# Kernel optimization log

Measured on AMD Instinct MI355X. Metric: run time of the kernel, lower is better.

Reference implementation:

```python
import jax, jax.numpy as jnp
import numpy as np

N, E, B = 50000, 200000, 64
IN_NODE, IN_EDGE = 64, 16
D_NODE, D_EDGE, HID, L = 128, 64, 64, 6


def _w(k, shape):
    # fan-in scaled init (like torch Linear default scale)
    return jax.random.normal(k, shape, jnp.float32) / np.sqrt(shape[-2]).astype(np.float32)


def setup_inputs() -> dict:
    key = jax.random.key(0)
    ks = jax.random.split(key, 16)
    return {
        "x": jax.random.normal(ks[0], (N, IN_NODE), jnp.float32),
        "edge_attr": jax.random.normal(ks[1], (E, IN_EDGE), jnp.float32),
        "edge_index": jax.random.randint(ks[2], (2, E), 0, N),
        "batch": jnp.sort(jax.random.randint(ks[3], (N,), 0, B)),
        "lin_x_w": _w(ks[4], (IN_NODE, D_NODE)), "lin_x_b": jnp.zeros((D_NODE,), jnp.float32),
        "lin_e_w": _w(ks[5], (IN_EDGE, D_EDGE)), "lin_e_b": jnp.zeros((D_EDGE,), jnp.float32),
        "msg_w": _w(ks[6], (L, D_NODE, D_EDGE)),
        "phie_w1": _w(ks[7], (L, D_EDGE + 2 * D_NODE, HID)), "phie_b1": jnp.zeros((L, HID), jnp.float32),
        "phie_w2": _w(ks[8], (L, HID, D_EDGE)), "phie_b2": jnp.zeros((L, D_EDGE), jnp.float32),
        "phiv_w1": _w(ks[9], (L, D_NODE + D_EDGE, HID)), "phiv_b1": jnp.zeros((L, HID), jnp.float32),
        "phiv_w2": _w(ks[10], (L, HID, D_NODE)), "phiv_b2": jnp.zeros((L, D_NODE), jnp.float32),
        "ro_w1": _w(ks[11], (D_NODE, D_NODE)), "ro_b1": jnp.zeros((D_NODE,), jnp.float32),
        "ro_w2": _w(ks[12], (D_NODE, D_NODE)), "ro_b2": jnp.zeros((D_NODE,), jnp.float32),
    }


def reference(x, edge_attr, edge_index, batch,
              lin_x_w, lin_x_b, lin_e_w, lin_e_b, msg_w,
              phie_w1, phie_b1, phie_w2, phie_b2,
              phiv_w1, phiv_b1, phiv_w2, phiv_b2,
              ro_w1, ro_b1, ro_w2, ro_b2):
    src, dst = edge_index[0], edge_index[1]
    n = x.shape[0]
    h = x @ lin_x_w + lin_x_b          # [N, d_node]
    e = edge_attr @ lin_e_w + lin_e_b  # [E, d_edge]
    # per-node in-degree for scatter_mean (clamped to 1, as in torch_scatter)
    deg = jnp.maximum(jax.ops.segment_sum(jnp.ones((dst.shape[0],), h.dtype), dst, num_segments=n), 1.0)[:, None]

    def step(carry, p):
        h, e = carry
        mw, ew1, eb1, ew2, eb2, vw1, vb1, vw2, vb2 = p
        hs, hd = h[src], h[dst]                       # gathers [E, d_node]
        e_in = jnp.concatenate([hs, hd, e + hs @ mw], axis=-1)  # [E, d_edge+2*d_node]
        e = e + jax.nn.relu(e_in @ ew1 + eb1) @ ew2 + eb2
        m_dst = jax.ops.segment_sum(e, dst, num_segments=n) / deg  # scatter_mean
        v_in = jnp.concatenate([h, m_dst], axis=-1)   # [N, d_node+d_edge]
        h = h + jax.nn.relu(v_in @ vw1 + vb1) @ vw2 + vb2
        return (h, e), None

    (h, e), _ = jax.lax.scan(step, (h, e),
                             (msg_w, phie_w1, phie_b1, phie_w2, phie_b2,
                              phiv_w1, phiv_b1, phiv_w2, phiv_b2))
    # graph readout: scatter_mean over batch assignment
    gcnt = jnp.maximum(jax.ops.segment_sum(jnp.ones((n,), h.dtype), batch, num_segments=B), 1.0)[:, None]
    graph_x = jax.ops.segment_sum(h, batch, num_segments=B) / gcnt  # [B, d_node]
    return jax.nn.relu(graph_x @ ro_w1 + ro_b1) @ ro_w2 + ro_b2
```

## Files before the change

kernel.cpp:

```cpp
#include <hip/hip_runtime.h>

constexpr int Nn  = 50000;
constexpr int Ne  = 200000;
constexpr int Bg  = 64;
constexpr int DN  = 128;
constexpr int DE  = 64;
constexpr int HD  = 64;
constexpr int INN = 64;
constexpr int INE = 16;
constexpr int LAY = 6;
constexpr int SB  = 196;

typedef __attribute__((ext_vector_type(8))) short sh8;
typedef __attribute__((ext_vector_type(4))) float f4;

__device__ inline unsigned short f2bf(float x) {
  union { float f; unsigned u; } v; v.f = x;
  unsigned r = v.u + 0x7FFF + ((v.u >> 16) & 1);
  return (unsigned short)(r >> 16);
}
__device__ inline float bf2f(unsigned short u) {
  union { unsigned u; float f; } v; v.u = ((unsigned)u) << 16; return v.f;
}
__device__ inline f4 mfma16(sh8 a, sh8 b, f4 c) {
  return __builtin_amdgcn_mfma_f32_16x16x32_bf16(a, b, c, 0, 0, 0);
}

__global__ void hist(const int* __restrict__ dst, int* __restrict__ deg) {
  const int j = blockIdx.x * blockDim.x + threadIdx.x;
  if (j < Ne) atomicAdd(&deg[dst[j]], 1);
}

__global__ __launch_bounds__(256) void scan1(const int* __restrict__ deg,
                                             int* __restrict__ rp,
                                             int* __restrict__ bsum) {
  __shared__ int s[256];
  const int t = threadIdx.x, i = blockIdx.x * 256 + t;
  const int v = (i < Nn) ? deg[i] : 0;
  s[t] = v; __syncthreads();
  for (int off = 1; off < 256; off <<= 1) {
    const int x = (t >= off) ? s[t - off] : 0;
    __syncthreads();
    s[t] += x;
    __syncthreads();
  }
  if (i < Nn) rp[i] = s[t] - v;
  if (t == 255) bsum[blockIdx.x] = s[255];
}

__global__ __launch_bounds__(256) void scan2(const int* __restrict__ bsum,
                                             int* __restrict__ boff) {
  __shared__ int s[256];
  const int t = threadIdx.x;
  const int v = (t < SB) ? bsum[t] : 0;
  s[t] = v; __syncthreads();
  for (int off = 1; off < 256; off <<= 1) {
    const int x = (t >= off) ? s[t - off] : 0;
    __syncthreads();
    s[t] += x;
    __syncthreads();
  }
  if (t < SB) boff[t] = s[t] - v;
}

__global__ __launch_bounds__(256) void scan3(int* __restrict__ rp,
                                             const int* __restrict__ boff,
                                             const int* __restrict__ deg,
                                             int* __restrict__ cursor,
                                             float* __restrict__ invdeg) {
  const int i = blockIdx.x * 256 + threadIdx.x;
  if (i < Nn) {
    const int r = rp[i] + boff[i >> 8];
    rp[i] = r;
    cursor[i] = r;
    invdeg[i] = 1.0f / fmaxf((float)deg[i], 1.0f);
  }
  if (i == 0) rp[Nn] = Ne;
}

__global__ void scatter(const int* __restrict__ src, const int* __restrict__ dst,
                        int* __restrict__ cursor, int* __restrict__ pos,
                        int* __restrict__ src_s, int* __restrict__ dst_s) {
  const int j = blockIdx.x * blockDim.x + threadIdx.x;
  if (j < Ne) {
    const int d = dst[j];
    const int p = atomicAdd(&cursor[d], 1);
    pos[j] = p;
    src_s[p] = src[j];
    dst_s[p] = d;
  }
}

__global__ __launch_bounds__(64) void prep_we(const float* __restrict__ ew1,
                                              const float* __restrict__ mw,
                                              const float* __restrict__ ew2,
                                              unsigned short* __restrict__ wpT,
                                              unsigned short* __restrict__ w1eT,
                                              unsigned short* __restrict__ ew2T) {
  const int l = blockIdx.x >> 6, n = blockIdx.x & 63, t = threadIdx.x;
  const float* E1 = ew1 + (long)l * 320 * 64;
  const float* MW = mw + (long)l * 128 * 64;
  const float* E2 = ew2 + (long)l * 64 * 64;
  unsigned short* WP = wpT + (long)l * 128 * 128;
  __shared__ float c[64];
  c[t] = E1[(256 + t) * 64 + n];
  __syncthreads();
  for (int k = t; k < 128; k += 64) {
    float s = E1[k * 64 + n];
    for (int j = 0; j < 64; ++j) s += MW[k * 64 + j] * c[j];
    WP[n * 128 + k] = f2bf(s);
    WP[(64 + n) * 128 + k] = f2bf(E1[(128 + k) * 64 + n]);
  }
  w1eT[(long)l * 64 * 64 + n * 64 + t] = f2bf(E1[(256 + t) * 64 + n]);
  ew2T[(long)l * 64 * 64 + n * 64 + t] = f2bf(E2[t * 64 + n]);
}

__global__ __launch_bounds__(64) void prep_wv(const float* __restrict__ vw1,
                                              const float* __restrict__ vw2,
                                              unsigned short* __restrict__ vw1T,
                                              unsigned short* __restrict__ vw2T) {
  const int l = blockIdx.x >> 7, n = blockIdx.x & 127, t = threadIdx.x;
  vw2T[(long)l * 128 * 64 + n * 64 + t] = f2bf(vw2[(long)l * 64 * 128 + t * 128 + n]);
  if (n < 64) {
    for (int k = t; k < 192; k += 64)
      vw1T[(long)l * 64 * 192 + n * 192 + k] = f2bf(vw1[(long)l * 192 * 64 + k * 64 + n]);
  }
}

__global__ __launch_bounds__(64) void prep_wx(const float* __restrict__ w,
                                              unsigned short* __restrict__ wxT) {
  const int n = blockIdx.x, t = threadIdx.x;
  wxT[n * INN + t] = f2bf(w[t * DN + n]);
}

__global__ __launch_bounds__(256) void enc_node_mfma(
    const float* __restrict__ x,
    const unsigned short* __restrict__ wxT,
    const float* __restrict__ b,
    unsigned short* __restrict__ hb) {
  const int lane = threadIdx.x & 63;
  const int wv   = threadIdx.x >> 6;
  const int quad = lane >> 4;
  const int lm   = lane & 15;
  const int wid  = blockIdx.x * 4 + wv;
  const int ntiles = (Nn + 31) / 32;
  if (wid >= ntiles) return;
  const int i0 = wid * 32;

  bool mv[2];
#pragma unroll
  for (int mt = 0; mt < 2; ++mt) mv[mt] = (i0 + mt * 16) < Nn;

  f4 acc[2][8];
#pragma unroll
  for (int mt = 0; mt < 2; ++mt)
#pragma unroll
    for (int nt = 0; nt < 8; ++nt) acc[mt][nt] = f4{0.f, 0.f, 0.f, 0.f};

#pragma unroll
  for (int ks = 0; ks < 2; ++ks) {
    const int kb = ks * 32 + quad * 8;
    sh8 a[2], bfr[8];
#pragma unroll
    for (int mt = 0; mt < 2; ++mt) {
      const int row = i0 + mt * 16 + lm;
      if (mv[mt] && row < Nn) {
        const float* xp = x + (long)row * INN + kb;
        const float4 v0 = *(const float4*)xp;
        const float4 v1 = *(const float4*)(xp + 4);
        a[mt][0] = (short)f2bf(v0.x); a[mt][1] = (short)f2bf(v0.y);
        a[mt][2] = (short)f2bf(v0.z); a[mt][3] = (short)f2bf(v0.w);
        a[mt][4] = (short)f2bf(v1.x); a[mt][5] = (short)f2bf(v1.y);
        a[mt][6] = (short)f2bf(v1.z); a[mt][7] = (short)f2bf(v1.w);
      } else a[mt] = (sh8)0;
    }
#pragma unroll
    for (int nt = 0; nt < 8; ++nt)
      bfr[nt] = *(const sh8*)(wxT + (nt * 16 + lm) * INN + kb);
#pragma unroll
    for (int mt = 0; mt < 2; ++mt)
#pragma unroll
      for (int nt = 0; nt < 8; ++nt)
        acc[mt][nt] = mfma16(a[mt], bfr[nt], acc[mt][nt]);
  }
  float bv[8];
#pragma unroll
  for (int nt = 0; nt < 8; ++nt) bv[nt] = b[nt * 16 + lm];
#pragma unroll
  for (int mt = 0; mt < 2; ++mt) {
    if (!mv[mt]) continue;
#pragma unroll
    for (int r = 0; r < 4; ++r) {
      const int row = i0 + mt * 16 + quad * 4 + r;
      if (row >= Nn) continue;
#pragma unroll
      for (int nt = 0; nt < 8; ++nt)
        hb[(long)row * DN + nt * 16 + lm] = f2bf(acc[mt][nt][r] + bv[nt]);
    }
  }
}

__global__ __launch_bounds__(256) void enc_edge(const float* __restrict__ ea,
                                                const int* __restrict__ pos,
                                                const float* __restrict__ w,
                                                const float* __restrict__ b,
                                                unsigned short* __restrict__ eb) {
  __shared__ float S[64 * INE];
  const int t = threadIdx.x;
  const int j0 = blockIdx.x * 64;
  *(float4*)&S[t * 4] = *(const float4*)&ea[(long)j0 * INE + t * 4];
  __syncthreads();
  const int lane = t & 63, wv = t >> 6;
  float wreg[INE];
#pragma unroll
  for (int k = 0; k < INE; ++k) wreg[k] = w[k * DE + lane];
  const float bias = b[lane];
#pragma unroll
  for (int el = 0; el < 16; ++el) {
    const int e = wv * 16 + el;
    float acc = bias;
#pragma unroll
    for (int k = 0; k < INE; ++k) acc += S[e * INE + k] * wreg[k];
    eb[(long)pos[j0 + e] * DE + lane] = f2bf(acc);
  }
}

constexpr int PP = 136;

__global__ __launch_bounds__(256) void proj_mfma(
    const unsigned short* __restrict__ hb,
    const unsigned short* __restrict__ wpT,
    unsigned short* __restrict__ P) {
  __shared__ unsigned short Us[4][32 * PP];
  const int lane = threadIdx.x & 63;
  const int wv   = threadIdx.x >> 6;
  const int quad = lane >> 4;
  const int lm   = lane & 15;
  const int kq   = quad * 8;
  const int wid  = blockIdx.x * 4 + wv;
  const int ntiles = (Nn + 31) / 32;
  if (wid >= ntiles) return;
  const int i0 = wid * 32;
  unsigned short* us = Us[wv];

  bool mv[2];
#pragma unroll
  for (int mt = 0; mt < 2; ++mt) mv[mt] = (i0 + mt * 16) < Nn;

  sh8 a[2][4];
#pragma unroll
  for (int mt = 0; mt < 2; ++mt) {
    const int row = i0 + mt * 16 + lm;
    if (mv[mt]) {
#pragma unroll
      for (int ks = 0; ks < 4; ++ks)
        a[mt][ks] = *(const sh8*)(hb + (long)row * DN + ks * 32 + kq);
    } else {
#pragma unroll
      for (int ks = 0; ks < 4; ++ks) a[mt][ks] = (sh8)0;
    }
  }

  f4 acc[2][8];
#pragma unroll
  for (int mt = 0; mt < 2; ++mt)
#pragma unroll
    for (int nt = 0; nt < 8; ++nt) acc[mt][nt] = f4{0.f, 0.f, 0.f, 0.f};

#pragma unroll
  for (int ks = 0; ks < 4; ++ks) {
    const int kb = ks * 32 + kq;
    sh8 bfr[8];
#pragma unroll
    for (int nt = 0; nt < 8; ++nt)
      bfr[nt] = *(const sh8*)(wpT + (nt * 16 + lm) * 128 + kb);
#pragma unroll
    for (int mt = 0; mt < 2; ++mt)
#pragma unroll
      for (int nt = 0; nt < 8; ++nt)
        acc[mt][nt] = mfma16(a[mt][ks], bfr[nt], acc[mt][nt]);
  }

#pragma unroll
  for (int mt = 0; mt < 2; ++mt)
#pragma unroll
    for (int nt = 0; nt < 8; ++nt)
#pragma unroll
      for (int r = 0; r < 4; ++r)
        us[(mt * 16 + quad * 4 + r) * PP + nt * 16 + lm] = f2bf(acc[mt][nt][r]);
#pragma unroll
  for (int s = 0; s < 8; ++s) {
    const int row = s * 4 + (lane >> 4);
    const int col8 = (lane & 15) * 8;
    if (i0 + row < Nn) {
      const sh8 v = *(const sh8*)&us[row * PP + col8];
      *(sh8*)(P + (long)(i0 + row) * 128 + col8) = v;
    }
  }
}

constexpr int UP = 72;

__global__ __launch_bounds__(256) void edge_layer_mfma(
    const unsigned short* __restrict__ P,
    unsigned short* __restrict__ eb,
    const int* __restrict__ src_s, const int* __restrict__ dst_s,
    const unsigned short* __restrict__ w1eT,
    const unsigned short* __restrict__ ew2T,
    const float* __restrict__ b1, const float* __restrict__ b2) {
  __shared__ unsigned short W1l[64 * UP];
  __shared__ unsigned short W2l[64 * UP];
  __shared__ unsigned short Us[4][32 * UP];
  const int t    = threadIdx.x;
  const int lane = t & 63;
  const int wv   = t >> 6;
  const int quad = lane >> 4;
  const int lm   = lane & 15;
  const int kq   = quad * 8;
  unsigned short* us = Us[wv];

#pragma unroll
  for (int c = 0; c < 2; ++c) {
    const int cc = c * 256 + t;
    const int n = cc >> 3, kc = (cc & 7) * 8;
    *(sh8*)&W1l[n * UP + kc] = *(const sh8*)(w1eT + n * 64 + kc);
    *(sh8*)&W2l[n * UP + kc] = *(const sh8*)(ew2T + n * 64 + kc);
  }
  __syncthreads();

  float b1v[4], b2v[4];
  sh8 bi[4];
#pragma unroll
  for (int nt = 0; nt < 4; ++nt) {
    b1v[nt] = b1[nt * 16 + lm];
    b2v[nt] = b2[nt * 16 + lm];
    const int d = nt * 16 + lm - (nt >> 1) * 32 - kq;
#pragma unroll
    for (int jj = 0; jj < 8; ++jj) bi[nt][jj] = (d == jj) ? (short)0x3F80 : (short)0;
  }

  const int ntiles = Ne / 32;
  const int nw = gridDim.x * 4;
  for (int wid = blockIdx.x * 4 + wv; wid < ntiles; wid += nw) {
    const int j0 = wid * 32;

    sh8 as_[2][2], ad_[2][2], ae_[2][2];
#pragma unroll
    for (int mt = 0; mt < 2; ++mt) {
      const int j = j0 + mt * 16 + lm;
      const long srow = (long)src_s[j] * 128;
      const long drow = (long)dst_s[j] * 128 + 64;
#pragma unroll
      for (int ks = 0; ks < 2; ++ks) {
        as_[mt][ks] = *(const sh8*)(P + srow + ks * 32 + kq);
        ad_[mt][ks] = *(const sh8*)(P + drow + ks * 32 + kq);
        ae_[mt][ks] = *(const sh8*)(eb + (long)j * DE + ks * 32 + kq);
      }
    }

    f4 acc[2][4];
#pragma unroll
    for (int mt = 0; mt < 2; ++mt)
#pragma unroll
      for (int nt = 0; nt < 4; ++nt) acc[mt][nt] = f4{0.f, 0.f, 0.f, 0.f};
#pragma unroll
    for (int ks = 0; ks < 2; ++ks) {
      const int kb = ks * 32 + kq;
      sh8 b[4];
#pragma unroll
      for (int nt = 0; nt < 4; ++nt)
        b[nt] = *(const sh8*)&W1l[(nt * 16 + lm) * UP + kb];
#pragma unroll
      for (int mt = 0; mt < 2; ++mt)
#pragma unroll
        for (int nt = 0; nt < 4; ++nt)
          acc[mt][nt] = mfma16(ae_[mt][ks], b[nt], acc[mt][nt]);
    }
#pragma unroll
    for (int nt = 0; nt < 4; ++nt)
#pragma unroll
      for (int mt = 0; mt < 2; ++mt) {
        acc[mt][nt] = mfma16(as_[mt][nt >> 1], bi[nt], acc[mt][nt]);
        acc[mt][nt] = mfma16(ad_[mt][nt >> 1], bi[nt], acc[mt][nt]);
      }

#pragma unroll
    for (int mt = 0; mt < 2; ++mt)
#pragma unroll
      for (int nt = 0; nt < 4; ++nt)
#pragma unroll
        for (int r = 0; r < 4; ++r) {
          const int row = mt * 16 + quad * 4 + r;
          const int col = nt * 16 + lm;
          us[row * UP + col] = f2bf(fmaxf(acc[mt][nt][r] + b1v[nt], 0.f));
        }

    f4 acc2[2][4];
#pragma unroll
    for (int mt = 0; mt < 2; ++mt)
#pragma unroll
      for (int nt = 0; nt < 4; ++nt) acc2[mt][nt] = f4{0.f, 0.f, 0.f, 0.f};
#pragma unroll
    for (int ks = 0; ks < 2; ++ks) {
      const int kb = ks * 32 + kq;
      sh8 au[2], b[4];
#pragma unroll
      for (int mt = 0; mt < 2; ++mt)
        au[mt] = *(const sh8*)&us[(mt * 16 + lm) * UP + kb];
#pragma unroll
      for (int nt = 0; nt < 4; ++nt)
        b[nt] = *(const sh8*)&W2l[(nt * 16 + lm) * UP + kb];
#pragma unroll
      for (int mt = 0; mt < 2; ++mt)
#pragma unroll
        for (int nt = 0; nt < 4; ++nt)
          acc2[mt][nt] = mfma16(au[mt], b[nt], acc2[mt][nt]);
    }
#pragma unroll
    for (int nt = 0; nt < 4; ++nt)
#pragma unroll
      for (int mt = 0; mt < 2; ++mt)
        acc2[mt][nt] = mfma16(ae_[mt][nt >> 1], bi[nt], acc2[mt][nt]);

#pragma unroll
    for (int mt = 0; mt < 2; ++mt)
#pragma unroll
      for (int nt = 0; nt < 4; ++nt)
#pragma unroll
        for (int r = 0; r < 4; ++r)
          us[(mt * 16 + quad * 4 + r) * UP + nt * 16 + lm] =
              f2bf(acc2[mt][nt][r] + b2v[nt]);
#pragma unroll
    for (int s = 0; s < 4; ++s) {
      const int row = s * 8 + (lane >> 3);
      const sh8 v = *(const sh8*)&us[row * UP + (lane & 7) * 8];
      *(sh8*)(eb + (long)(j0 + row) * DE + (lane & 7) * 8) = v;
    }
  }
}

constexpr int VP1 = 200;
constexpr int VP2 = 72;
constexpr int V2OFF = 64 * VP1;

__global__ __launch_bounds__(256) void node_layer_mfma(
    unsigned short* __restrict__ hb,
    const unsigned short* __restrict__ eb,
    const int* __restrict__ rp,
    const float* __restrict__ invdeg,
    const unsigned short* __restrict__ vw1T,
    const unsigned short* __restrict__ vw2T,
    const float* __restrict__ b1, const float* __restrict__ b2) {
  __shared__ unsigned short Wl[64 * VP1 + 128 * VP2];
  __shared__ unsigned short Us[4][32 * UP];
  const int t    = threadIdx.x;
  const int lane = t & 63;
  const int wv   = t >> 6;
  const int quad = lane >> 4;
  const int lm   = lane & 15;
  const int kq   = quad * 8;
  unsigned short* us = Us[wv];

#pragma unroll
  for (int c = 0; c < 6; ++c) {
    const int cc = c * 256 + t;
    const int n = cc / 24, kc = (cc % 24) * 8;
    *(sh8*)&Wl[n * VP1 + kc] = *(const sh8*)(vw1T + n * 192 + kc);
  }
#pragma unroll
  for (int c = 0; c < 4; ++c) {
    const int cc = c * 256 + t;
    const int n = cc / 8, kc = (cc % 8) * 8;
    *(sh8*)&Wl[V2OFF + n * VP2 + kc] = *(const sh8*)(vw2T + n * 64 + kc);
  }
  __syncthreads();

  float b1v[4];
  sh8 bi[4];
#pragma unroll
  for (int nt = 0; nt < 4; ++nt) {
    b1v[nt] = b1[nt * 16 + lm];
    const int d = nt * 16 + lm - (nt >> 1) * 32 - kq;
#pragma unroll
    for (int jj = 0; jj < 8; ++jj) bi[nt][jj] = (d == jj) ? (short)0x3F80 : (short)0;
  }
  float b2v[2][4];
#pragma unroll
  for (int nh = 0; nh < 2; ++nh)
#pragma unroll
    for (int nt = 0; nt < 4; ++nt) b2v[nh][nt] = b2[nh * 64 + nt * 16 + lm];

  const int ntiles = (Nn + 31) / 32;
  const int nw = gridDim.x * 4;
  for (int wid = blockIdx.x * 4 + wv; wid < ntiles; wid += nw) {
    const int i0 = wid * 32;
    bool mv[2];
#pragma unroll
    for (int mt = 0; mt < 2; ++mt) mv[mt] = (i0 + mt * 16) < Nn;

    sh8 a[2][6];
#pragma unroll
    for (int mt = 0; mt < 2; ++mt) {
      const int row = i0 + mt * 16 + lm;
      if (mv[mt]) {
#pragma unroll
        for (int ks = 0; ks < 4; ++ks)
          a[mt][ks] = *(const sh8*)(hb + (long)row * DN + ks * 32 + kq);
        const int js = rp[row], je = rp[row + 1];
        float m0[8], m1[8];
#pragma unroll
        for (int c = 0; c < 8; ++c) { m0[c] = 0.f; m1[c] = 0.f; }
        for (int j = js; j < je; ++j) {
          const sh8 v0 = *(const sh8*)(eb + (long)j * DE + kq);
          const sh8 v1 = *(const sh8*)(eb + (long)j * DE + 32 + kq);
#pragma unroll
          for (int c = 0; c < 8; ++c) {
            m0[c] += bf2f((unsigned short)v0[c]);
            m1[c] += bf2f((unsigned short)v1[c]);
          }
        }
        const float inv = invdeg[row];
        sh8 f0, f1;
#pragma unroll
        for (int c = 0; c < 8; ++c) {
          f0[c] = (short)f2bf(m0[c] * inv);
          f1[c] = (short)f2bf(m1[c] * inv);
        }
        a[mt][4] = f0;
        a[mt][5] = f1;
      } else {
#pragma unroll
        for (int ks = 0; ks < 6; ++ks) a[mt][ks] = (sh8)0;
      }
    }

    f4 acc[2][4];
#pragma unroll
    for (int mt = 0; mt < 2; ++mt)
#pragma unroll
      for (int nt = 0; nt < 4; ++nt) acc[mt][nt] = f4{0.f, 0.f, 0.f, 0.f};
#pragma unroll
    for (int ks = 0; ks < 6; ++ks) {
      const int kb = ks * 32 + kq;
      sh8 b[4];
#pragma unroll
      for (int nt = 0; nt < 4; ++nt)
        b[nt] = *(const sh8*)&Wl[(nt * 16 + lm) * VP1 + kb];
#pragma unroll
      for (int mt = 0; mt < 2; ++mt)
#pragma unroll
        for (int nt = 0; nt < 4; ++nt)
          acc[mt][nt] = mfma16(a[mt][ks], b[nt], acc[mt][nt]);
    }
#pragma unroll
    for (int mt = 0; mt < 2; ++mt)
#pragma unroll
      for (int nt = 0; nt < 4; ++nt)
#pragma unroll
        for (int r = 0; r < 4; ++r) {
          const int row = mt * 16 + quad * 4 + r;
          const int col = nt * 16 + lm;
          us[row * UP + col] = f2bf(fmaxf(acc[mt][nt][r] + b1v[nt], 0.f));
        }

    sh8 au[2][2];
#pragma unroll
    for (int ks = 0; ks < 2; ++ks)
#pragma unroll
      for (int mt = 0; mt < 2; ++mt)
        au[mt][ks] = *(const sh8*)&us[(mt * 16 + lm) * UP + ks * 32 + kq];

#pragma unroll
    for (int nh = 0; nh < 2; ++nh) {
      f4 acc2[2][4];
#pragma unroll
      for (int mt = 0; mt < 2; ++mt)
#pragma unroll
        for (int nt = 0; nt < 4; ++nt) acc2[mt][nt] = f4{0.f, 0.f, 0.f, 0.f};
#pragma unroll
      for (int ks = 0; ks < 2; ++ks) {
        const int kb = ks * 32 + kq;
        sh8 b[4];
#pragma unroll
        for (int nt = 0; nt < 4; ++nt)
          b[nt] = *(const sh8*)&Wl[V2OFF + (nh * 64 + nt * 16 + lm) * VP2 + kb];
#pragma unroll
        for (int mt = 0; mt < 2; ++mt)
#pragma unroll
          for (int nt = 0; nt < 4; ++nt)
            acc2[mt][nt] = mfma16(au[mt][ks], b[nt], acc2[mt][nt]);
      }
#pragma unroll
      for (int nt = 0; nt < 4; ++nt)
#pragma unroll
        for (int mt = 0; mt < 2; ++mt)
          acc2[mt][nt] = mfma16(a[mt][nh * 2 + (nt >> 1)], bi[nt], acc2[mt][nt]);

#pragma unroll
      for (int mt = 0; mt < 2; ++mt)
#pragma unroll
        for (int nt = 0; nt < 4; ++nt)
#pragma unroll
          for (int r = 0; r < 4; ++r)
            us[(mt * 16 + quad * 4 + r) * UP + nt * 16 + lm] =
                f2bf(acc2[mt][nt][r] + b2v[nh][nt]);
#pragma unroll
      for (int s = 0; s < 4; ++s) {
        const int row = s * 8 + (lane >> 3);
        if (i0 + row < Nn) {
          const sh8 v = *(const sh8*)&us[row * UP + (lane & 7) * 8];
          *(sh8*)(hb + (long)(i0 + row) * DN + nh * 64 + (lane & 7) * 8) = v;
        }
      }
    }
  }
}

constexpr int GB = 512;

__global__ __launch_bounds__(128) void graph_acc(const unsigned short* __restrict__ hb,
                                                 const int* __restrict__ batch,
                                                 float* __restrict__ gacc,
                                                 float* __restrict__ gcnt) {
  const int c = threadIdx.x;
  const int per = (Nn + GB - 1) / GB;
  const int s0 = blockIdx.x * per;
  const int s1 = min(s0 + per, Nn);
  if (s0 >= s1) return;
  int cur = batch[s0];
  float acc = 0.f, cnt = 0.f;
  for (int i = s0; i < s1; ++i) {
    const int b = batch[i];
    if (b != cur) {
      atomicAdd(&gacc[cur * DN + c], acc);
      if (c == 0) atomicAdd(&gcnt[cur], cnt);
      acc = 0.f; cnt = 0.f; cur = b;
    }
    acc += bf2f(hb[(long)i * DN + c]);
    cnt += 1.f;
  }
  atomicAdd(&gacc[cur * DN + c], acc);
  if (c == 0) atomicAdd(&gcnt[cur], cnt);
}

__global__ __launch_bounds__(128) void readout(const float* __restrict__ gacc,
                                               const float* __restrict__ gcnt,
                                               const float* __restrict__ w1,
                                               const float* __restrict__ b1,
                                               const float* __restrict__ w2,
                                               const float* __restrict__ b2,
                                               float* __restrict__ out) {
  __shared__ float g[DN], t1[DN];
  const int b = blockIdx.x, c = threadIdx.x;
  const float inv = 1.0f / fmaxf(gcnt[b], 1.0f);
  g[c] = gacc[b * DN + c] * inv;
  __syncthreads();
  float acc = b1[c];
  for (int k = 0; k < DN; ++k) acc += g[k] * w1[k * DN + c];
  t1[c] = fmaxf(acc, 0.0f);
  __syncthreads();
  acc = b2[c];
  for (int k = 0; k < DN; ++k) acc += t1[k] * w2[k * DN + c];
  out[b * DN + c] = acc;
}

extern "C" void kernel_launch(void* const* d_in, const int* in_sizes, int n_in,
                              void* d_out, int out_size, void* d_ws, size_t ws_size,
                              hipStream_t stream) {
  const float* x       = (const float*)d_in[0];
  const float* ea      = (const float*)d_in[1];
  const int*   ei      = (const int*)d_in[2];
  const int*   batch   = (const int*)d_in[3];
  const float* lin_x_w = (const float*)d_in[4];
  const float* lin_x_b = (const float*)d_in[5];
  const float* lin_e_w = (const float*)d_in[6];
  const float* lin_e_b = (const float*)d_in[7];
  const float* msg_w   = (const float*)d_in[8];
  const float* phie_w1 = (const float*)d_in[9];
  const float* phie_b1 = (const float*)d_in[10];
  const float* phie_w2 = (const float*)d_in[11];
  const float* phie_b2 = (const float*)d_in[12];
  const float* phiv_w1 = (const float*)d_in[13];
  const float* phiv_b1 = (const float*)d_in[14];
  const float* phiv_w2 = (const float*)d_in[15];
  const float* phiv_b2 = (const float*)d_in[16];
  const float* ro_w1   = (const float*)d_in[17];
  const float* ro_b1   = (const float*)d_in[18];
  const float* ro_w2   = (const float*)d_in[19];
  const float* ro_b2   = (const float*)d_in[20];

  const int* srcp = ei;
  const int* dstp = ei + Ne;

  int*   deg_i  = (int*)d_ws;
  float* gacc   = (float*)(deg_i + Nn);
  float* gcnt   = gacc + Bg * DN;
  float* invdeg = gcnt + Bg;
  int*   row_ptr= (int*)(invdeg + Nn);
  int*   cursor = row_ptr + Nn + 8;
  int*   bsum   = cursor + Nn;
  int*   boff   = bsum + 256;
  int*   pos    = boff + 256;
  int*   src_s  = pos + Ne;
  int*   dst_s  = src_s + Ne;
  unsigned short* hb   = (unsigned short*)(dst_s + Ne);
  unsigned short* eb   = hb + (long)Nn * DN;
  unsigned short* Pm   = eb + (long)Ne * DE;
  unsigned short* wpT  = Pm + (long)Nn * 128;
  unsigned short* w1eT = wpT + (long)LAY * 128 * 128;
  unsigned short* ew2T = w1eT + (long)LAY * 64 * 64;
  unsigned short* vw1T = ew2T + (long)LAY * 64 * 64;
  unsigned short* vw2T = vw1T + (long)LAY * 64 * 192;
  unsigned short* wxT  = vw2T + (long)LAY * 128 * 64;

  hipMemsetAsync(deg_i, 0, sizeof(int) * Nn + sizeof(float) * (Bg * DN + Bg), stream);

  hist<<<(Ne + 255) / 256, 256, 0, stream>>>(dstp, deg_i);
  scan1<<<SB, 256, 0, stream>>>(deg_i, row_ptr, bsum);
  scan2<<<1, 256, 0, stream>>>(bsum, boff);
  scan3<<<SB, 256, 0, stream>>>(row_ptr, boff, deg_i, cursor, invdeg);
  scatter<<<(Ne + 255) / 256, 256, 0, stream>>>(srcp, dstp, cursor, pos, src_s, dst_s);

  prep_we<<<LAY * 64, 64, 0, stream>>>(phie_w1, msg_w, phie_w2, wpT, w1eT, ew2T);
  prep_wv<<<LAY * 128, 64, 0, stream>>>(phiv_w1, phiv_w2, vw1T, vw2T);
  prep_wx<<<DN, 64, 0, stream>>>(lin_x_w, wxT);

  const int tblocks = ((Nn + 31) / 32 + 3) / 4;
  enc_node_mfma<<<tblocks, 256, 0, stream>>>(x, wxT, lin_x_b, hb);
  enc_edge<<<Ne / 64, 256, 0, stream>>>(ea, pos, lin_e_w, lin_e_b, eb);

  const int eblocks = 1024;
  const int vblocks = 512;

  for (int l = 0; l < LAY; ++l) {
    proj_mfma<<<tblocks, 256, 0, stream>>>(hb, wpT + (long)l * 128 * 128, Pm);
    edge_layer_mfma<<<eblocks, 256, 0, stream>>>(
        Pm, eb, src_s, dst_s,
        w1eT + (long)l * 64 * 64, ew2T + (long)l * 64 * 64,
        phie_b1 + (long)l * HD, phie_b2 + (long)l * DE);
    node_layer_mfma<<<vblocks, 256, 0, stream>>>(
        hb, eb, row_ptr, invdeg,
        vw1T + (long)l * 64 * 192, vw2T + (long)l * 128 * 64,
        phiv_b1 + (long)l * HD, phiv_b2 + (long)l * DN);
  }

  graph_acc<<<GB, 128, 0, stream>>>(hb, batch, gacc, gcnt);
  readout<<<Bg, 128, 0, stream>>>(gacc, gcnt, ro_w1, ro_b1, ro_w2, ro_b2,
                                  (float*)d_out);
}
```

Baseline: 518.0 us.

## Fuse per-layer node projection into node encoder and node-update kernels

```diff
diff --git a/kernel.cpp b/kernel.cpp
--- a/kernel.cpp
+++ b/kernel.cpp
@@ -133,19 +133,26 @@
   wxT[n * INN + t] = f2bf(w[t * DN + n]);
 }
 
+constexpr int PP = 136;
+
 __global__ __launch_bounds__(256) void enc_node_mfma(
     const float* __restrict__ x,
     const unsigned short* __restrict__ wxT,
     const float* __restrict__ b,
-    unsigned short* __restrict__ hb) {
+    unsigned short* __restrict__ hb,
+    const unsigned short* __restrict__ wp0,
+    unsigned short* __restrict__ P) {
+  __shared__ unsigned short Us[4][32 * PP];
   const int lane = threadIdx.x & 63;
   const int wv   = threadIdx.x >> 6;
   const int quad = lane >> 4;
   const int lm   = lane & 15;
+  const int kq   = quad * 8;
   const int wid  = blockIdx.x * 4 + wv;
   const int ntiles = (Nn + 31) / 32;
   if (wid >= ntiles) return;
   const int i0 = wid * 32;
+  unsigned short* us = Us[wv];
 
   bool mv[2];
 #pragma unroll
@@ -159,7 +166,7 @@
 
 #pragma unroll
   for (int ks = 0; ks < 2; ++ks) {
-    const int kb = ks * 32 + quad * 8;
+    const int kb = ks * 32 + kq;
     sh8 a[2], bfr[8];
 #pragma unroll
     for (int mt = 0; mt < 2; ++mt) {
@@ -186,16 +193,65 @@
   float bv[8];
 #pragma unroll
   for (int nt = 0; nt < 8; ++nt) bv[nt] = b[nt * 16 + lm];
-#pragma unroll
-  for (int mt = 0; mt < 2; ++mt) {
-    if (!mv[mt]) continue;
-#pragma unroll
-    for (int r = 0; r < 4; ++r) {
-      const int row = i0 + mt * 16 + quad * 4 + r;
-      if (row >= Nn) continue;
+
+#pragma unroll
+  for (int mt = 0; mt < 2; ++mt)
+#pragma unroll
+    for (int nt = 0; nt < 8; ++nt)
+#pragma unroll
+      for (int r = 0; r < 4; ++r)
+        us[(mt * 16 + quad * 4 + r) * PP + nt * 16 + lm] =
+            f2bf(acc[mt][nt][r] + bv[nt]);
+
+#pragma unroll
+  for (int s = 0; s < 8; ++s) {
+    const int row = s * 4 + (lane >> 4);
+    const int col8 = (lane & 15) * 8;
+    if (i0 + row < Nn) {
+      const sh8 v = *(const sh8*)&us[row * PP + col8];
+      *(sh8*)(hb + (long)(i0 + row) * DN + col8) = v;
+    }
+  }
+
+  sh8 ah[2][4];
+#pragma unroll
+  for (int mt = 0; mt < 2; ++mt)
+#pragma unroll
+    for (int ks = 0; ks < 4; ++ks)
+      ah[mt][ks] = *(const sh8*)&us[(mt * 16 + lm) * PP + ks * 32 + kq];
+
+  f4 accp[2][8];
+#pragma unroll
+  for (int mt = 0; mt < 2; ++mt)
+#pragma unroll
+    for (int nt = 0; nt < 8; ++nt) accp[mt][nt] = f4{0.f, 0.f, 0.f, 0.f};
+#pragma unroll
+  for (int ks = 0; ks < 4; ++ks) {
+    const int kb = ks * 32 + kq;
+    sh8 bfr[8];
+#pragma unroll
+    for (int nt = 0; nt < 8; ++nt)
+      bfr[nt] = *(const sh8*)(wp0 + (nt * 16 + lm) * 128 + kb);
+#pragma unroll
+    for (int mt = 0; mt < 2; ++mt)
 #pragma unroll
       for (int nt = 0; nt < 8; ++nt)
-        hb[(long)row * DN + nt * 16 + lm] = f2bf(acc[mt][nt][r] + bv[nt]);
+        accp[mt][nt] = mfma16(ah[mt][ks], bfr[nt], accp[mt][nt]);
+  }
+#pragma unroll
+  for (int mt = 0; mt < 2; ++mt)
+#pragma unroll
+    for (int nt = 0; nt < 8; ++nt)
+#pragma unroll
+      for (int r = 0; r < 4; ++r)
+        us[(mt * 16 + quad * 4 + r) * PP + nt * 16 + lm] = f2bf(accp[mt][nt][r]);
+#pragma unroll
+  for (int s = 0; s < 8; ++s) {
+    const int row = s * 4 + (lane >> 4);
+    const int col8 = (lane & 15) * 8;
+    if (i0 + row < Nn) {
+      const sh8 v = *(const sh8*)&us[row * PP + col8];
+      *(sh8*)(P + (long)(i0 + row) * 128 + col8) = v;
     }
   }
 }
@@ -222,80 +278,6 @@
 #pragma unroll
     for (int k = 0; k < INE; ++k) acc += S[e * INE + k] * wreg[k];
     eb[(long)pos[j0 + e] * DE + lane] = f2bf(acc);
-  }
-}
-
-constexpr int PP = 136;
-
-__global__ __launch_bounds__(256) void proj_mfma(
-    const unsigned short* __restrict__ hb,
-    const unsigned short* __restrict__ wpT,
-    unsigned short* __restrict__ P) {
-  __shared__ unsigned short Us[4][32 * PP];
-  const int lane = threadIdx.x & 63;
-  const int wv   = threadIdx.x >> 6;
-  const int quad = lane >> 4;
-  const int lm   = lane & 15;
-  const int kq   = quad * 8;
-  const int wid  = blockIdx.x * 4 + wv;
-  const int ntiles = (Nn + 31) / 32;
-  if (wid >= ntiles) return;
-  const int i0 = wid * 32;
-  unsigned short* us = Us[wv];
-
-  bool mv[2];
-#pragma unroll
-  for (int mt = 0; mt < 2; ++mt) mv[mt] = (i0 + mt * 16) < Nn;
-
-  sh8 a[2][4];
-#pragma unroll
-  for (int mt = 0; mt < 2; ++mt) {
-    const int row = i0 + mt * 16 + lm;
-    if (mv[mt]) {
-#pragma unroll
-      for (int ks = 0; ks < 4; ++ks)
-        a[mt][ks] = *(const sh8*)(hb + (long)row * DN + ks * 32 + kq);
-    } else {
-#pragma unroll
-      for (int ks = 0; ks < 4; ++ks) a[mt][ks] = (sh8)0;
-    }
-  }
-
-  f4 acc[2][8];
-#pragma unroll
-  for (int mt = 0; mt < 2; ++mt)
-#pragma unroll
-    for (int nt = 0; nt < 8; ++nt) acc[mt][nt] = f4{0.f, 0.f, 0.f, 0.f};
-
-#pragma unroll
-  for (int ks = 0; ks < 4; ++ks) {
-    const int kb = ks * 32 + kq;
-    sh8 bfr[8];
-#pragma unroll
-    for (int nt = 0; nt < 8; ++nt)
-      bfr[nt] = *(const sh8*)(wpT + (nt * 16 + lm) * 128 + kb);
-#pragma unroll
-    for (int mt = 0; mt < 2; ++mt)
-#pragma unroll
-      for (int nt = 0; nt < 8; ++nt)
-        acc[mt][nt] = mfma16(a[mt][ks], bfr[nt], acc[mt][nt]);
-  }
-
-#pragma unroll
-  for (int mt = 0; mt < 2; ++mt)
-#pragma unroll
-    for (int nt = 0; nt < 8; ++nt)
-#pragma unroll
-      for (int r = 0; r < 4; ++r)
-        us[(mt * 16 + quad * 4 + r) * PP + nt * 16 + lm] = f2bf(acc[mt][nt][r]);
-#pragma unroll
-  for (int s = 0; s < 8; ++s) {
-    const int row = s * 4 + (lane >> 4);
-    const int col8 = (lane & 15) * 8;
-    if (i0 + row < Nn) {
-      const sh8 v = *(const sh8*)&us[row * PP + col8];
-      *(sh8*)(P + (long)(i0 + row) * 128 + col8) = v;
-    }
   }
 }
 
@@ -450,16 +432,18 @@
     const float* __restrict__ invdeg,
     const unsigned short* __restrict__ vw1T,
     const unsigned short* __restrict__ vw2T,
-    const float* __restrict__ b1, const float* __restrict__ b2) {
+    const float* __restrict__ b1, const float* __restrict__ b2,
+    const unsigned short* __restrict__ wp_next,
+    unsigned short* __restrict__ P) {
   __shared__ unsigned short Wl[64 * VP1 + 128 * VP2];
-  __shared__ unsigned short Us[4][32 * UP];
+  __shared__ unsigned short Hs[4][32 * PP];
   const int t    = threadIdx.x;
   const int lane = t & 63;
   const int wv   = t >> 6;
   const int quad = lane >> 4;
   const int lm   = lane & 15;
   const int kq   = quad * 8;
-  unsigned short* us = Us[wv];
+  unsigned short* us = Hs[wv];
 
 #pragma unroll
   for (int c = 0; c < 6; ++c) {
@@ -560,7 +544,7 @@
         for (int r = 0; r < 4; ++r) {
           const int row = mt * 16 + quad * 4 + r;
           const int col = nt * 16 + lm;
-          us[row * UP + col] = f2bf(fmaxf(acc[mt][nt][r] + b1v[nt], 0.f));
+          us[row * PP + col] = f2bf(fmaxf(acc[mt][nt][r] + b1v[nt], 0.f));
         }
 
     sh8 au[2][2];
@@ -568,7 +552,7 @@
     for (int ks = 0; ks < 2; ++ks)
 #pragma unroll
       for (int mt = 0; mt < 2; ++mt)
-        au[mt][ks] = *(const sh8*)&us[(mt * 16 + lm) * UP + ks * 32 + kq];
+        au[mt][ks] = *(const sh8*)&us[(mt * 16 + lm) * PP + ks * 32 + kq];
 
 #pragma unroll
     for (int nh = 0; nh < 2; ++nh) {
@@ -602,14 +586,61 @@
         for (int nt = 0; nt < 4; ++nt)
 #pragma unroll
           for (int r = 0; r < 4; ++r)
-            us[(mt * 16 + quad * 4 + r) * UP + nt * 16 + lm] =
+            us[(mt * 16 + quad * 4 + r) * PP + nh * 64 + nt * 16 + lm] =
                 f2bf(acc2[mt][nt][r] + b2v[nh][nt]);
-#pragma unroll
-      for (int s = 0; s < 4; ++s) {
-        const int row = s * 8 + (lane >> 3);
+    }
+
+#pragma unroll
+    for (int s = 0; s < 8; ++s) {
+      const int row = s * 4 + (lane >> 4);
+      const int col8 = (lane & 15) * 8;
+      if (i0 + row < Nn) {
+        const sh8 v = *(const sh8*)&us[row * PP + col8];
+        *(sh8*)(hb + (long)(i0 + row) * DN + col8) = v;
+      }
+    }
+
+    if (wp_next) {
+      sh8 ah[2][4];
+#pragma unroll
+      for (int mt = 0; mt < 2; ++mt)
+#pragma unroll
+        for (int ks = 0; ks < 4; ++ks)
+          ah[mt][ks] = *(const sh8*)&us[(mt * 16 + lm) * PP + ks * 32 + kq];
+
+      f4 accp[2][8];
+#pragma unroll
+      for (int mt = 0; mt < 2; ++mt)
+#pragma unroll
+        for (int nt = 0; nt < 8; ++nt) accp[mt][nt] = f4{0.f, 0.f, 0.f, 0.f};
+#pragma unroll
+      for (int ks = 0; ks < 4; ++ks) {
+        const int kb = ks * 32 + kq;
+        sh8 bfr[8];
+#pragma unroll
+        for (int nt = 0; nt < 8; ++nt)
+          bfr[nt] = *(const sh8*)(wp_next + (nt * 16 + lm) * 128 + kb);
+#pragma unroll
+        for (int mt = 0; mt < 2; ++mt)
+#pragma unroll
+          for (int nt = 0; nt < 8; ++nt)
+            accp[mt][nt] = mfma16(ah[mt][ks], bfr[nt], accp[mt][nt]);
+      }
+#pragma unroll
+      for (int mt = 0; mt < 2; ++mt)
+#pragma unroll
+        for (int nt = 0; nt < 8; ++nt)
+#pragma unroll
+          for (int r = 0; r < 4; ++r)
+            us[(mt * 16 + quad * 4 + r) * PP + nt * 16 + lm] =
+                f2bf(accp[mt][nt][r]);
+#pragma unroll
+      for (int s = 0; s < 8; ++s) {
+        const int row = s * 4 + (lane >> 4);
+        const int col8 = (lane & 15) * 8;
         if (i0 + row < Nn) {
-          const sh8 v = *(const sh8*)&us[row * UP + (lane & 7) * 8];
-          *(sh8*)(hb + (long)(i0 + row) * DN + nh * 64 + (lane & 7) * 8) = v;
+          const sh8 v = *(const sh8*)&us[row * PP + col8];
+          *(sh8*)(P + (long)(i0 + row) * 128 + col8) = v;
         }
       }
     }
@@ -726,22 +757,24 @@
   prep_wx<<<DN, 64, 0, stream>>>(lin_x_w, wxT);
 
   const int tblocks = ((Nn + 31) / 32 + 3) / 4;
-  enc_node_mfma<<<tblocks, 256, 0, stream>>>(x, wxT, lin_x_b, hb);
+  enc_node_mfma<<<tblocks, 256, 0, stream>>>(x, wxT, lin_x_b, hb, wpT, Pm);
   enc_edge<<<Ne / 64, 256, 0, stream>>>(ea, pos, lin_e_w, lin_e_b, eb);
 
   const int eblocks = 1024;
   const int vblocks = 512;
 
   for (int l = 0; l < LAY; ++l) {
-    proj_mfma<<<tblocks, 256, 0, stream>>>(hb, wpT + (long)l * 128 * 128, Pm);
     edge_layer_mfma<<<eblocks, 256, 0, stream>>>(
         Pm, eb, src_s, dst_s,
         w1eT + (long)l * 64 * 64, ew2T + (long)l * 64 * 64,
         phie_b1 + (long)l * HD, phie_b2 + (long)l * DE);
+    const unsigned short* wp_next =
+        (l + 1 < LAY) ? (wpT + (long)(l + 1) * 128 * 128) : nullptr;
     node_layer_mfma<<<vblocks, 256, 0, stream>>>(
         hb, eb, row_ptr, invdeg,
         vw1T + (long)l * 64 * 192, vw2T + (long)l * 128 * 64,
-        phiv_b1 + (long)l * HD, phiv_b2 + (long)l * DN);
+        phiv_b1 + (long)l * HD, phiv_b2 + (long)l * DN,
+        wp_next, Pm);
   }
 
   graph_acc<<<GB, 128, 0, stream>>>(hb, batch, gacc, gcnt);
```

Result: slower. 540.8 us (+4.4%).
